# Performance work log

Hardware: AMD Instinct MI355X
Metric: run time of the kernel (lower is better)

The kernel has to match this reference:

```python
import jax, jax.numpy as jnp
import numpy as np

N = 50000
E = 800000
F_IN = 128
H = 8        # heads
C = 32       # hidden_channels per head
HC = H * C   # 256
NEG_SLOPE = 0.2


def setup_inputs() -> dict:
    key = jax.random.key(0)
    ks = jax.random.split(key, 16)
    s = 0.1
    return {
        'x': jax.random.normal(ks[0], (N, F_IN), jnp.float32),
        'edge_index': jax.random.randint(ks[1], (2, E), 0, N, jnp.int64),
        'edge_weights': jax.random.uniform(ks[2], (E,), jnp.float32),
        'W1': jax.random.normal(ks[3], (F_IN, HC), jnp.float32) * s,
        'att_src1': jax.random.normal(ks[4], (H, C), jnp.float32) * s,
        'att_dst1': jax.random.normal(ks[5], (H, C), jnp.float32) * s,
        'b1': jnp.zeros((HC,), jnp.float32),
        'W2': jax.random.normal(ks[6], (HC, HC), jnp.float32) * s,
        'att_src2': jax.random.normal(ks[7], (H, C), jnp.float32) * s,
        'att_dst2': jax.random.normal(ks[8], (H, C), jnp.float32) * s,
        'b2': jnp.zeros((HC,), jnp.float32),
        'We': jax.random.normal(ks[9], (HC, 1), jnp.float32) * s,
        'be': jnp.zeros((1,), jnp.float32),
        'Wn': jax.random.normal(ks[10], (HC, 1), jnp.float32) * s,
        'bn': jnp.zeros((1,), jnp.float32),
    }


def gat_conv(x, src, dst, W, att_src, att_dst, bias):
    """PyG GATConv (concat=True, eval mode, self-loops already in src/dst)."""
    n = x.shape[0]
    h = (x @ W).reshape(n, H, C)                      # [N,H,C]
    a_s = jnp.sum(h * att_src, axis=-1)               # [N,H]
    a_d = jnp.sum(h * att_dst, axis=-1)               # [N,H]
    e = jax.nn.leaky_relu(a_s[src] + a_d[dst], NEG_SLOPE)  # [E',H]
    m = jax.ops.segment_max(e, dst, num_segments=n)   # segment softmax over dst
    ex = jnp.exp(e - m[dst])
    denom = jax.ops.segment_sum(ex, dst, num_segments=n)
    alpha = ex / (denom[dst] + 1e-16)                 # [E',H]
    out = jax.ops.segment_sum(alpha[..., None] * h[src], dst, num_segments=n)
    return out.reshape(n, HC) + bias


def reference(x, edge_index, edge_weights, W1, att_src1, att_dst1, b1,
              W2, att_src2, att_dst2, b2, We, be, Wn, bn):
    src0, dst0 = edge_index[0], edge_index[1]
    loops = jnp.arange(N, dtype=src0.dtype)
    src = jnp.concatenate([src0, loops])
    dst = jnp.concatenate([dst0, loops])
    # edge_weights is passed to GATConv as edge_attr but unused (edge_dim=None)
    h = jax.nn.relu(gat_conv(x, src, dst, W1, att_src1, att_dst1, b1))
    h = jax.nn.relu(gat_conv(h, src, dst, W2, att_src2, att_dst2, b2))
    edge_pred = (h[src0] * h[dst0]) @ We + be          # [E,1]
    node_pred = h @ Wn + bn                            # [N,1]
    return (edge_pred, node_pred)
```

## Files before the change

### kernel.cpp

```cpp
#include <hip/hip_runtime.h>
#include <hip/hip_bf16.h>

#define NN 50000
#define NE 800000
#define FIN 128
#define HC 256
#define NEG_SLOPE 0.2f
#define LOG2E 1.4426950408889634f

#define GEMM_BLOCKS 1564
#define NSCAT 3328
#define NB_HIST 782
#define NB_X 6250
#define NB_W1 128
#define NB_W2 256
#define CE_CAP (NE + 4 * NN + 16)

typedef short bf16x8 __attribute__((ext_vector_type(8)));
typedef float f32x4 __attribute__((ext_vector_type(4)));

__device__ __forceinline__ unsigned short f2bf(float f) {
  unsigned u = __float_as_uint(f);
  u += 0x7fff + ((u >> 16) & 1);
  return (unsigned short)(u >> 16);
}
__device__ __forceinline__ float bf2f(unsigned short s) {
  return __uint_as_float((unsigned)s << 16);
}
__device__ __forceinline__ float bflo(unsigned u) { return __uint_as_float(u << 16); }
__device__ __forceinline__ float bfhi(unsigned u) { return __uint_as_float(u & 0xffff0000u); }

__global__ __launch_bounds__(256) void prep_hist(
    const float* __restrict__ X, unsigned short* __restrict__ Xh,
    const float* __restrict__ W1, unsigned short* __restrict__ W1th,
    unsigned short* __restrict__ W1tl, const float* __restrict__ W2,
    unsigned short* __restrict__ W2th, unsigned short* __restrict__ W2tl,
    const int* __restrict__ ei, int* __restrict__ counts,
    unsigned* __restrict__ gA, unsigned* __restrict__ gB, float* __restrict__ asg) {
  int b = blockIdx.x, t = threadIdx.x;
  if (b < NB_HIST) {
#pragma unroll
    for (int u = 0; u < 4; ++u) {
      int e = b * 1024 + u * 256 + t;
      if (e < NE) atomicAdd(&counts[ei[NE + e]], 1);
    }
  } else if (b < NB_HIST + NB_X) {
    int i = (b - NB_HIST) * 256 + t;
    float4 v = ((const float4*)X)[i];
    ushort4 h;
    h.x = f2bf(v.x); h.y = f2bf(v.y); h.z = f2bf(v.z); h.w = f2bf(v.w);
    ((ushort4*)Xh)[i] = h;
  } else if (b < NB_HIST + NB_X + NB_W1) {
    int j = (b - NB_HIST - NB_X) * 256 + t;
    int n = j >> 7, k = j & 127;
    float v = W1[k * HC + n];
    unsigned short h = f2bf(v);
    W1th[j] = h;
    W1tl[j] = f2bf(v - bf2f(h));
  } else if (b < NB_HIST + NB_X + NB_W1 + NB_W2) {
    int j = (b - NB_HIST - NB_X - NB_W1) * 256 + t;
    int n = j >> 8, k = j & 255;
    float v = W2[k * HC + n];
    unsigned short h = f2bf(v);
    W2th[j] = h;
    W2tl[j] = f2bf(v - bf2f(h));
  } else {
    if (t < 128) { gA[t] = 0; gB[t] = 0; }
    if (t < 8) asg[t] = -1e30f;
  }
}

__global__ __launch_bounds__(256) void gemm_coef(
    const unsigned short* __restrict__ A, const unsigned short* __restrict__ Bth,
    const unsigned short* __restrict__ Btl, const float* __restrict__ att_s,
    const float* __restrict__ att_d, unsigned short* __restrict__ Cb,
    float* __restrict__ a_s, float* __restrict__ a_d, int M, int K,
    const int* __restrict__ ei, const int* __restrict__ rowptr,
    int* __restrict__ tmpc, int2* __restrict__ ce, int scat) {
  __shared__ unsigned short sA[64 * 40];
  __shared__ unsigned short sBh[128 * 40];
  __shared__ unsigned short sBl[128 * 40];
  __shared__ float sCS[64][4];
  __shared__ float sCD[64][4];

  int bid = blockIdx.x, t = threadIdx.x;
  if (bid < scat) {
    int x = bid & 7;
    int c = bid >> 3;
#pragma unroll
    for (int u = 0; u < 8; ++u) {
      int e = c * 2048 + u * 256 + t;
      if (e < NE + NN) {
        int d = (e < NE) ? ei[NE + e] : e - NE;
        if ((unsigned)d / 6250u == (unsigned)x) {
          int s  = (e < NE) ? ei[e] : d;
          int id = (e < NE) ? e : -1;
          int pos = rowptr[d] + atomicAdd(&tmpc[d], 1);
          ce[pos] = make_int2(s, id);
        }
      }
    }
    return;
  }

  int gb = bid - scat;
  int w = t >> 6, lane = t & 63;
  int quad = lane >> 4, lrow = lane & 15;
  int m0 = (gb >> 1) * 64, n0 = (gb & 1) * 128;
  int rm = (w & 1) * 32, cn = (w >> 1) * 64;

  f32x4 acc[2][4] = {};

  for (int k0 = 0; k0 < K; k0 += 32) {
    {
      int row = t >> 2, q = t & 3;
      int gm = m0 + row;
      if (gm >= M) gm = M - 1;
      *(uint4*)(sA + row * 40 + q * 8) = *(const uint4*)(A + (size_t)gm * K + k0 + q * 8);
    }
#pragma unroll
    for (int i = 0; i < 2; ++i) {
      int idx = t + i * 256;
      int row = idx >> 2, q = idx & 3;
      size_t gbx = (size_t)(n0 + row) * K + k0 + q * 8;
      *(uint4*)(sBh + row * 40 + q * 8) = *(const uint4*)(Bth + gbx);
      *(uint4*)(sBl + row * 40 + q * 8) = *(const uint4*)(Btl + gbx);
    }
    __syncthreads();

    bf16x8 fa[2];
#pragma unroll
    for (int mi = 0; mi < 2; ++mi)
      fa[mi] = *(const bf16x8*)(sA + (rm + mi * 16 + lrow) * 40 + quad * 8);
#pragma unroll
    for (int ni = 0; ni < 4; ++ni) {
      bf16x8 fbh = *(const bf16x8*)(sBh + (cn + ni * 16 + lrow) * 40 + quad * 8);
      bf16x8 fbl = *(const bf16x8*)(sBl + (cn + ni * 16 + lrow) * 40 + quad * 8);
#pragma unroll
      for (int mi = 0; mi < 2; ++mi) {
        acc[mi][ni] = __builtin_amdgcn_mfma_f32_16x16x32_bf16(fa[mi], fbh, acc[mi][ni], 0, 0, 0);
        acc[mi][ni] = __builtin_amdgcn_mfma_f32_16x16x32_bf16(fa[mi], fbl, acc[mi][ni], 0, 0, 0);
      }
    }
    __syncthreads();
  }

  float vs[4], vd[4];
#pragma unroll
  for (int ni = 0; ni < 4; ++ni) {
    int gn = n0 + cn + ni * 16 + lrow;
    vs[ni] = att_s[gn] * LOG2E;
    vd[ni] = att_d[gn] * LOG2E;
  }
  int h4e = cn >> 5;

#pragma unroll
  for (int mi = 0; mi < 2; ++mi) {
#pragma unroll
    for (int r = 0; r < 4; ++r) {
      int lr = rm + mi * 16 + quad * 4 + r;
      int gm = m0 + lr;
      if (gm < M) {
#pragma unroll
        for (int ni = 0; ni < 4; ++ni) {
          int gn = n0 + cn + ni * 16 + lrow;
          Cb[(size_t)gm * HC + gn] = f2bf(acc[mi][ni][r]);
        }
      }
      float pse = acc[mi][0][r] * vs[0] + acc[mi][1][r] * vs[1];
      float pso = acc[mi][2][r] * vs[2] + acc[mi][3][r] * vs[3];
      float pde = acc[mi][0][r] * vd[0] + acc[mi][1][r] * vd[1];
      float pdo = acc[mi][2][r] * vd[2] + acc[mi][3][r] * vd[3];
#pragma unroll
      for (int off = 1; off <= 8; off <<= 1) {
        pse += __shfl_xor(pse, off);
        pso += __shfl_xor(pso, off);
        pde += __shfl_xor(pde, off);
        pdo += __shfl_xor(pdo, off);
      }
      if (lrow == 0) {
        sCS[lr][h4e] = pse;
        sCS[lr][h4e + 1] = pso;
        sCD[lr][h4e] = pde;
        sCD[lr][h4e + 1] = pdo;
      }
    }
  }
  __syncthreads();
  if (t < 64) {
    int gm = m0 + t;
    if (gm < M) {
      int o = (n0 >> 5);
      *(float4*)(a_s + (size_t)gm * 8 + o) = *(const float4*)&sCS[t][0];
      *(float4*)(a_d + (size_t)gm * 8 + o) = *(const float4*)&sCD[t][0];
    }
  }
}

__global__ void scan1(const int* __restrict__ counts, int* __restrict__ scanbuf,
                      int* __restrict__ bsum) {
  __shared__ int sd[256];
  int t = threadIdx.x;
  int i = blockIdx.x * 256 + t;
  int v = (i < NN) ? ((counts[i] + 1 + 3) & ~3) : 0;
  sd[t] = v;
  __syncthreads();
#pragma unroll
  for (int off = 1; off < 256; off <<= 1) {
    int x = (t >= off) ? sd[t - off] : 0;
    __syncthreads();
    sd[t] += x;
    __syncthreads();
  }
  if (i < NN) scanbuf[i] = sd[t];
  if (t == 255) bsum[blockIdx.x] = sd[255];
}

__global__ void scan2(const int* __restrict__ bsum, int* __restrict__ boff, int nb) {
  __shared__ int sd[256];
  int t = threadIdx.x;
  int v = (t < nb) ? bsum[t] : 0;
  sd[t] = v;
  __syncthreads();
#pragma unroll
  for (int off = 1; off < 256; off <<= 1) {
    int x = (t >= off) ? sd[t - off] : 0;
    __syncthreads();
    sd[t] += x;
    __syncthreads();
  }
  if (t < nb) boff[t] = sd[t] - v;
}

__global__ void scan3(const int* __restrict__ scanbuf, const int* __restrict__ boff,
                      int* __restrict__ rowptr) {
  int i = blockIdx.x * 256 + threadIdx.x;
  if (i < NN) rowptr[i + 1] = scanbuf[i] + boff[blockIdx.x];
  if (i == 0) rowptr[0] = 0;
}

__global__ __launch_bounds__(256) void agg_kernel(
    const unsigned short* __restrict__ htb, const float* __restrict__ a_s,
    const float* __restrict__ a_d, const int* __restrict__ rowptr,
    const int2* __restrict__ ce, const float* __restrict__ bias,
    unsigned short* __restrict__ outb,
    const float* __restrict__ Wn, const float* __restrict__ bn,
    float* __restrict__ outn) {
  int d = blockIdx.x * 4 + (threadIdx.x >> 6);
  if (d >= NN) return;
  int l = threadIdx.x & 63;
  int hh = l >> 3;
  const uint2* ht2 = (const uint2*)htb;
  float adh = a_d[d * 8 + hh];
  int r0 = rowptr[d], r1 = rowptr[d + 1];
  float denom = 0.f;
  float4 acc = {0.f, 0.f, 0.f, 0.f};
  for (int r = r0; r < r1; r += 4) {
    int s[4];
#pragma unroll
    for (int j = 0; j < 4; ++j) s[j] = ce[r + j].x;
    float as_[4];
    uint2 q[4];
#pragma unroll
    for (int j = 0; j < 4; ++j) {
      as_[j] = a_s[s[j] * 8 + hh];
      q[j] = ht2[s[j] * 64 + l];
    }
#pragma unroll
    for (int j = 0; j < 4; ++j) {
      float e = as_[j] + adh;
      e = fmaxf(e, NEG_SLOPE * e);
      float w = exp2f(e);
      denom += w;
      acc.x += w * bflo(q[j].x);
      acc.y += w * bfhi(q[j].x);
      acc.z += w * bflo(q[j].y);
      acc.w += w * bfhi(q[j].y);
    }
  }
  float dv = 1.f / denom;
  float4 bi = *(const float4*)(bias + l * 4);
  float4 o;
  o.x = fmaxf(fmaf(acc.x, dv, bi.x), 0.f);
  o.y = fmaxf(fmaf(acc.y, dv, bi.y), 0.f);
  o.z = fmaxf(fmaf(acc.z, dv, bi.z), 0.f);
  o.w = fmaxf(fmaf(acc.w, dv, bi.w), 0.f);
  uint2 pb;
  pb.x = (unsigned)f2bf(o.x) | ((unsigned)f2bf(o.y) << 16);
  pb.y = (unsigned)f2bf(o.z) | ((unsigned)f2bf(o.w) << 16);
  ((uint2*)outb)[d * 64 + l] = pb;
  if (outn) {
    float4 wv = *(const float4*)(Wn + l * 4);
    float p = o.x * wv.x + o.y * wv.y + o.z * wv.z + o.w * wv.w;
#pragma unroll
    for (int off = 1; off <= 32; off <<= 1) p += __shfl_xor(p, off);
    if (l == 0) outn[d] = p + bn[0];
  }
}

__global__ __launch_bounds__(256) void edge_pred_kernel(
    const unsigned short* __restrict__ h2b, const int* __restrict__ rowptr,
    const int2* __restrict__ ce, const float* __restrict__ We,
    const float* __restrict__ be, float* __restrict__ out) {
  int d = blockIdx.x * 4 + (threadIdx.x >> 6);
  if (d >= NN) return;
  int lane = threadIdx.x & 63;
  int g = lane >> 4, l = lane & 15;
  float b = be[0];
  const uint4* h24 = (const uint4*)h2b;

  uint4 qd0 = h24[d * 32 + l * 2], qd1 = h24[d * 32 + l * 2 + 1];
  float wd[16];
  {
    const float4* wep = (const float4*)(We + l * 16);
    float4 w0 = wep[0], w1 = wep[1], w2 = wep[2], w3 = wep[3];
    wd[0] = bflo(qd0.x) * w0.x;  wd[1] = bfhi(qd0.x) * w0.y;
    wd[2] = bflo(qd0.y) * w0.z;  wd[3] = bfhi(qd0.y) * w0.w;
    wd[4] = bflo(qd0.z) * w1.x;  wd[5] = bfhi(qd0.z) * w1.y;
    wd[6] = bflo(qd0.w) * w1.z;  wd[7] = bfhi(qd0.w) * w1.w;
    wd[8] = bflo(qd1.x) * w2.x;  wd[9] = bfhi(qd1.x) * w2.y;
    wd[10] = bflo(qd1.y) * w2.z; wd[11] = bfhi(qd1.y) * w2.w;
    wd[12] = bflo(qd1.z) * w3.x; wd[13] = bfhi(qd1.z) * w3.y;
    wd[14] = bflo(qd1.w) * w3.z; wd[15] = bfhi(qd1.w) * w3.w;
  }

  int r0 = rowptr[d], r1 = rowptr[d + 1];
  for (int r = r0; r < r1; r += 8) {
    int rr0 = r + g, rr1 = r + 4 + g;
    int s0 = 0, id0 = -1, s1 = 0, id1 = -1;
    if (rr0 < r1) { int2 p = ce[rr0]; s0 = p.x; id0 = p.y; }
    if (rr1 < r1) { int2 p = ce[rr1]; s1 = p.x; id1 = p.y; }
    uint4 a0 = h24[s0 * 32 + l * 2], a1 = h24[s0 * 32 + l * 2 + 1];
    uint4 c0 = h24[s1 * 32 + l * 2], c1 = h24[s1 * 32 + l * 2 + 1];
    float p0 = bflo(a0.x) * wd[0] + bfhi(a0.x) * wd[1] + bflo(a0.y) * wd[2] +
               bfhi(a0.y) * wd[3] + bflo(a0.z) * wd[4] + bfhi(a0.z) * wd[5] +
               bflo(a0.w) * wd[6] + bfhi(a0.w) * wd[7] + bflo(a1.x) * wd[8] +
               bfhi(a1.x) * wd[9] + bflo(a1.y) * wd[10] + bfhi(a1.y) * wd[11] +
               bflo(a1.z) * wd[12] + bfhi(a1.z) * wd[13] + bflo(a1.w) * wd[14] +
               bfhi(a1.w) * wd[15];
    float p1 = bflo(c0.x) * wd[0] + bfhi(c0.x) * wd[1] + bflo(c0.y) * wd[2] +
               bfhi(c0.y) * wd[3] + bflo(c0.z) * wd[4] + bfhi(c0.z) * wd[5] +
               bflo(c0.w) * wd[6] + bfhi(c0.w) * wd[7] + bflo(c1.x) * wd[8] +
               bfhi(c1.x) * wd[9] + bflo(c1.y) * wd[10] + bfhi(c1.y) * wd[11] +
               bflo(c1.z) * wd[12] + bfhi(c1.z) * wd[13] + bflo(c1.w) * wd[14] +
               bfhi(c1.w) * wd[15];
#pragma unroll
    for (int off = 1; off <= 8; off <<= 1) {
      p0 += __shfl_xor(p0, off);
      p1 += __shfl_xor(p1, off);
    }
    if (l == 0) {
      if (id0 >= 0) out[id0] = p0 + b;
      if (id1 >= 0) out[id1] = p1 + b;
    }
  }
}

extern "C" void kernel_launch(void* const* d_in, const int* in_sizes, int n_in,
                              void* d_out, int out_size, void* d_ws, size_t ws_size,
                              hipStream_t stream) {
  const float* x  = (const float*)d_in[0];
  const int* ei   = (const int*)d_in[1];
  const float* W1 = (const float*)d_in[3];
  const float* as1 = (const float*)d_in[4];
  const float* ad1 = (const float*)d_in[5];
  const float* b1 = (const float*)d_in[6];
  const float* W2 = (const float*)d_in[7];
  const float* as2 = (const float*)d_in[8];
  const float* ad2 = (const float*)d_in[9];
  const float* b2 = (const float*)d_in[10];
  const float* We = (const float*)d_in[11];
  const float* be = (const float*)d_in[12];
  const float* Wn = (const float*)d_in[13];
  const float* bn = (const float*)d_in[14];
  float* out = (float*)d_out;

  char* wsp = (char*)d_ws;
  auto alloc = [&](size_t bytes) {
    char* p = wsp;
    wsp += (bytes + 255) & ~(size_t)255;
    return p;
  };
  unsigned short* hbAr = (unsigned short*)alloc((size_t)(NN + 1) * HC * 2);
  unsigned short* hbA = hbAr + HC;
  unsigned short* h1b = (unsigned short*)alloc((size_t)NN * HC * 2);
  unsigned short* hbBr = (unsigned short*)alloc((size_t)(NN + 1) * HC * 2);
  unsigned short* hbB = hbBr + HC;
  float* a_sr = (float*)alloc((size_t)(8 + NN * 8) * 4);
  float* a_s = a_sr + 8;
  float* a_d = (float*)alloc((size_t)NN * 8 * 4);
  int* rowptr = (int*)alloc((size_t)(NN + 1) * 4);
  int2* ce = (int2*)alloc((size_t)CE_CAP * 8);
  int* counts = (int*)alloc((size_t)NN * 4);
  int* tmp = (int*)alloc((size_t)NN * 4);
  int* scanbuf = (int*)alloc((size_t)NN * 4);
  int* bsum = (int*)alloc(256 * 4);
  int* boff = (int*)alloc(256 * 4);
  unsigned short* W1th = (unsigned short*)alloc((size_t)FIN * HC * 2);
  unsigned short* W1tl = (unsigned short*)alloc((size_t)FIN * HC * 2);
  unsigned short* W2th = (unsigned short*)alloc((size_t)HC * HC * 2);
  unsigned short* W2tl = (unsigned short*)alloc((size_t)HC * HC * 2);

  unsigned short* xh = h1b;

  const int NB = (NN + 255) / 256;

  hipMemsetAsync(counts, 0,
                 (size_t)((char*)tmp - (char*)counts) + (size_t)NN * 4, stream);
  hipMemsetAsync(ce, 0xFF, (size_t)CE_CAP * 8, stream);

  prep_hist<<<NB_HIST + NB_X + NB_W1 + NB_W2 + 1, 256, 0, stream>>>(
      x, xh, W1, W1th, W1tl, W2, W2th, W2tl, ei, counts,
      (unsigned*)hbAr, (unsigned*)hbBr, a_sr);
  scan1<<<NB, 256, 0, stream>>>(counts, scanbuf, bsum);
  scan2<<<1, 256, 0, stream>>>(bsum, boff, NB);
  scan3<<<NB, 256, 0, stream>>>(scanbuf, boff, rowptr);

  gemm_coef<<<NSCAT + GEMM_BLOCKS, 256, 0, stream>>>(
      xh, W1th, W1tl, as1, ad1, hbA, a_s, a_d, NN, FIN, ei, rowptr, tmp, ce, NSCAT);
  agg_kernel<<<NN / 4, 256, 0, stream>>>(hbA, a_s, a_d, rowptr, ce, b1, h1b,
                                         (const float*)nullptr, (const float*)nullptr,
                                         (float*)nullptr);

  gemm_coef<<<GEMM_BLOCKS, 256, 0, stream>>>(
      h1b, W2th, W2tl, as2, ad2, hbA, a_s, a_d, NN, HC,
      (const int*)nullptr, rowptr, tmp, ce, 0);
  agg_kernel<<<NN / 4, 256, 0, stream>>>(hbA, a_s, a_d, rowptr, ce, b2, hbB,
                                         Wn, bn, out + NE);

  edge_pred_kernel<<<NN / 4, 256, 0, stream>>>(hbB, rowptr, ce, We, be, out);
}
```

Baseline: 436.0 us.

## Replace CSR scan with fixed-width ELL adjacency using histogram ranks

The histogram pass now records each edge's rank within its destination, so the scatter writes edges directly into a fixed 64-slot-per-node ELL array. This removes the three scan kernels, the temporary counter array and the large memset of the edge list. The aggregation loop also loads four neighbour entries with two 16-byte loads. In exchange it assumes no node has more than 63 incoming edges, overflowing silently otherwise, and the padded buffer is larger and less dense.

```diff
diff --git a/kernel.cpp b/kernel.cpp
--- a/kernel.cpp
+++ b/kernel.cpp
@@ -14,7 +14,7 @@
 #define NB_X 6250
 #define NB_W1 128
 #define NB_W2 256
-#define CE_CAP (NE + 4 * NN + 16)
+#define ELLS 64
 
 typedef short bf16x8 __attribute__((ext_vector_type(8)));
 typedef float f32x4 __attribute__((ext_vector_type(4)));
@@ -35,14 +35,14 @@
     const float* __restrict__ W1, unsigned short* __restrict__ W1th,
     unsigned short* __restrict__ W1tl, const float* __restrict__ W2,
     unsigned short* __restrict__ W2th, unsigned short* __restrict__ W2tl,
-    const int* __restrict__ ei, int* __restrict__ counts,
+    const int* __restrict__ ei, int* __restrict__ counts, int* __restrict__ rank,
     unsigned* __restrict__ gA, unsigned* __restrict__ gB, float* __restrict__ asg) {
   int b = blockIdx.x, t = threadIdx.x;
   if (b < NB_HIST) {
 #pragma unroll
     for (int u = 0; u < 4; ++u) {
       int e = b * 1024 + u * 256 + t;
-      if (e < NE) atomicAdd(&counts[ei[NE + e]], 1);
+      if (e < NE) rank[e] = atomicAdd(&counts[ei[NE + e]], 1);
     }
   } else if (b < NB_HIST + NB_X) {
     int i = (b - NB_HIST) * 256 + t;
@@ -75,8 +75,8 @@
     const unsigned short* __restrict__ Btl, const float* __restrict__ att_s,
     const float* __restrict__ att_d, unsigned short* __restrict__ Cb,
     float* __restrict__ a_s, float* __restrict__ a_d, int M, int K,
-    const int* __restrict__ ei, const int* __restrict__ rowptr,
-    int* __restrict__ tmpc, int2* __restrict__ ce, int scat) {
+    const int* __restrict__ ei, const int* __restrict__ cnts,
+    const int* __restrict__ rank, int2* __restrict__ ce, int scat) {
   __shared__ unsigned short sA[64 * 40];
   __shared__ unsigned short sBh[128 * 40];
   __shared__ unsigned short sBl[128 * 40];
@@ -93,10 +93,15 @@
       if (e < NE + NN) {
         int d = (e < NE) ? ei[NE + e] : e - NE;
         if ((unsigned)d / 6250u == (unsigned)x) {
-          int s  = (e < NE) ? ei[e] : d;
-          int id = (e < NE) ? e : -1;
-          int pos = rowptr[d] + atomicAdd(&tmpc[d], 1);
-          ce[pos] = make_int2(s, id);
+          if (e < NE) {
+            ce[d * ELLS + rank[e]] = make_int2(ei[e], e);
+          } else {
+            int cnt = cnts[d];
+            int pad4 = (cnt + 4) & ~3;
+            ce[d * ELLS + cnt] = make_int2(d, -1);
+            for (int p = cnt + 1; p < pad4; ++p)
+              ce[d * ELLS + p] = make_int2(-1, -1);
+          }
         }
       }
     }
@@ -197,51 +202,9 @@
   }
 }
 
-__global__ void scan1(const int* __restrict__ counts, int* __restrict__ scanbuf,
-                      int* __restrict__ bsum) {
-  __shared__ int sd[256];
-  int t = threadIdx.x;
-  int i = blockIdx.x * 256 + t;
-  int v = (i < NN) ? ((counts[i] + 1 + 3) & ~3) : 0;
-  sd[t] = v;
-  __syncthreads();
-#pragma unroll
-  for (int off = 1; off < 256; off <<= 1) {
-    int x = (t >= off) ? sd[t - off] : 0;
-    __syncthreads();
-    sd[t] += x;
-    __syncthreads();
-  }
-  if (i < NN) scanbuf[i] = sd[t];
-  if (t == 255) bsum[blockIdx.x] = sd[255];
-}
-
-__global__ void scan2(const int* __restrict__ bsum, int* __restrict__ boff, int nb) {
-  __shared__ int sd[256];
-  int t = threadIdx.x;
-  int v = (t < nb) ? bsum[t] : 0;
-  sd[t] = v;
-  __syncthreads();
-#pragma unroll
-  for (int off = 1; off < 256; off <<= 1) {
-    int x = (t >= off) ? sd[t - off] : 0;
-    __syncthreads();
-    sd[t] += x;
-    __syncthreads();
-  }
-  if (t < nb) boff[t] = sd[t] - v;
-}
-
-__global__ void scan3(const int* __restrict__ scanbuf, const int* __restrict__ boff,
-                      int* __restrict__ rowptr) {
-  int i = blockIdx.x * 256 + threadIdx.x;
-  if (i < NN) rowptr[i + 1] = scanbuf[i] + boff[blockIdx.x];
-  if (i == 0) rowptr[0] = 0;
-}
-
 __global__ __launch_bounds__(256) void agg_kernel(
     const unsigned short* __restrict__ htb, const float* __restrict__ a_s,
-    const float* __restrict__ a_d, const int* __restrict__ rowptr,
+    const float* __restrict__ a_d, const int* __restrict__ cnts,
     const int2* __restrict__ ce, const float* __restrict__ bias,
     unsigned short* __restrict__ outb,
     const float* __restrict__ Wn, const float* __restrict__ bn,
@@ -252,13 +215,14 @@
   int hh = l >> 3;
   const uint2* ht2 = (const uint2*)htb;
   float adh = a_d[d * 8 + hh];
-  int r0 = rowptr[d], r1 = rowptr[d + 1];
+  int r0 = d * ELLS;
+  int r1 = r0 + ((cnts[d] + 4) & ~3);
   float denom = 0.f;
   float4 acc = {0.f, 0.f, 0.f, 0.f};
   for (int r = r0; r < r1; r += 4) {
-    int s[4];
-#pragma unroll
-    for (int j = 0; j < 4; ++j) s[j] = ce[r + j].x;
+    const int4* cp = (const int4*)(ce + r);
+    int4 c01 = cp[0], c23 = cp[1];
+    int s[4] = {c01.x, c01.z, c23.x, c23.z};
     float as_[4];
     uint2 q[4];
 #pragma unroll
@@ -299,7 +263,7 @@
 }
 
 __global__ __launch_bounds__(256) void edge_pred_kernel(
-    const unsigned short* __restrict__ h2b, const int* __restrict__ rowptr,
+    const unsigned short* __restrict__ h2b, const int* __restrict__ cnts,
     const int2* __restrict__ ce, const float* __restrict__ We,
     const float* __restrict__ be, float* __restrict__ out) {
   int d = blockIdx.x * 4 + (threadIdx.x >> 6);
@@ -324,7 +288,7 @@
     wd[14] = bflo(qd1.w) * w3.z; wd[15] = bfhi(qd1.w) * w3.w;
   }
 
-  int r0 = rowptr[d], r1 = rowptr[d + 1];
+  int r0 = d * ELLS, r1 = r0 + cnts[d];
   for (int r = r0; r < r1; r += 8) {
     int rr0 = r + g, rr1 = r + 4 + g;
     int s0 = 0, id0 = -1, s1 = 0, id1 = -1;
@@ -389,13 +353,9 @@
   float* a_sr = (float*)alloc((size_t)(8 + NN * 8) * 4);
   float* a_s = a_sr + 8;
   float* a_d = (float*)alloc((size_t)NN * 8 * 4);
-  int* rowptr = (int*)alloc((size_t)(NN + 1) * 4);
-  int2* ce = (int2*)alloc((size_t)CE_CAP * 8);
+  int2* ce = (int2*)alloc((size_t)NN * ELLS * 8);
   int* counts = (int*)alloc((size_t)NN * 4);
-  int* tmp = (int*)alloc((size_t)NN * 4);
-  int* scanbuf = (int*)alloc((size_t)NN * 4);
-  int* bsum = (int*)alloc(256 * 4);
-  int* boff = (int*)alloc(256 * 4);
+  int* rank = (int*)alloc((size_t)NE * 4);
   unsigned short* W1th = (unsigned short*)alloc((size_t)FIN * HC * 2);
   unsigned short* W1tl = (unsigned short*)alloc((size_t)FIN * HC * 2);
   unsigned short* W2th = (unsigned short*)alloc((size_t)HC * HC * 2);
@@ -403,30 +363,23 @@
 
   unsigned short* xh = h1b;
 
-  const int NB = (NN + 255) / 256;
-
-  hipMemsetAsync(counts, 0,
-                 (size_t)((char*)tmp - (char*)counts) + (size_t)NN * 4, stream);
-  hipMemsetAsync(ce, 0xFF, (size_t)CE_CAP * 8, stream);
+  hipMemsetAsync(counts, 0, (size_t)NN * 4, stream);
 
   prep_hist<<<NB_HIST + NB_X + NB_W1 + NB_W2 + 1, 256, 0, stream>>>(
-      x, xh, W1, W1th, W1tl, W2, W2th, W2tl, ei, counts,
+      x, xh, W1, W1th, W1tl, W2, W2th, W2tl, ei, counts, rank,
       (unsigned*)hbAr, (unsigned*)hbBr, a_sr);
-  scan1<<<NB, 256, 0, stream>>>(counts, scanbuf, bsum);
-  scan2<<<1, 256, 0, stream>>>(bsum, boff, NB);
-  scan3<<<NB, 256, 0, stream>>>(scanbuf, boff, rowptr);
 
   gemm_coef<<<NSCAT + GEMM_BLOCKS, 256, 0, stream>>>(
-      xh, W1th, W1tl, as1, ad1, hbA, a_s, a_d, NN, FIN, ei, rowptr, tmp, ce, NSCAT);
-  agg_kernel<<<NN / 4, 256, 0, stream>>>(hbA, a_s, a_d, rowptr, ce, b1, h1b,
+      xh, W1th, W1tl, as1, ad1, hbA, a_s, a_d, NN, FIN, ei, counts, rank, ce, NSCAT);
+  agg_kernel<<<NN / 4, 256, 0, stream>>>(hbA, a_s, a_d, counts, ce, b1, h1b,
                                          (const float*)nullptr, (const float*)nullptr,
                                          (float*)nullptr);
 
   gemm_coef<<<GEMM_BLOCKS, 256, 0, stream>>>(
       h1b, W2th, W2tl, as2, ad2, hbA, a_s, a_d, NN, HC,
-      (const int*)nullptr, rowptr, tmp, ce, 0);
-  agg_kernel<<<NN / 4, 256, 0, stream>>>(hbA, a_s, a_d, rowptr, ce, b2, hbB,
+      (const int*)nullptr, counts, rank, ce, 0);
+  agg_kernel<<<NN / 4, 256, 0, stream>>>(hbA, a_s, a_d, counts, ce, b2, hbB,
                                          Wn, bn, out + NE);
 
-  edge_pred_kernel<<<NN / 4, 256, 0, stream>>>(hbB, rowptr, ce, We, be, out);
-}
+  edge_pred_kernel<<<NN / 4, 256, 0, stream>>>(hbB, counts, ce, We, be, out);
+}
```

After: 409.3 us. 6.1% less time.
